# Kernel tuning notes

Hardware: AMD Instinct MI355X
Metric: run time of the kernel (lower is better)

## Reference

```python
import jax, jax.numpy as jnp
import numpy as np

NUM_EMBEDDINGS = 1024
EMBEDDING_DIM = 256
COMMITMENT_COST = 0.25
B = 65536


def setup_inputs() -> dict:
    key = jax.random.key(0)
    k1, k2 = jax.random.split(key)
    inputs = jax.random.normal(k1, (B, EMBEDDING_DIM), dtype=jnp.float32)
    # torch init: uniform(-1/K, 1/K)
    W = jax.random.uniform(k2, (NUM_EMBEDDINGS, EMBEDDING_DIM), dtype=jnp.float32,
                           minval=-1.0 / NUM_EMBEDDINGS, maxval=1.0 / NUM_EMBEDDINGS)
    return {"inputs": inputs, "W": W}


def reference(inputs, W):
    x = inputs  # (B, D)
    # squared L2 distances to every codebook entry: (B, K)
    distances = (jnp.sum(x * x, axis=1, keepdims=True)
                 + jnp.sum(W * W, axis=1)
                 - 2.0 * jnp.matmul(x, W.T))
    idx = jnp.argmin(distances, axis=1)  # (B,)
    # one-hot @ W is just a gather
    quantized = jnp.take(W, idx, axis=0)  # (B, D)

    sg = jax.lax.stop_gradient
    e_latent_loss = jnp.mean((sg(quantized) - x) ** 2)
    q_latent_loss = jnp.mean((quantized - sg(x)) ** 2)
    loss = q_latent_loss + COMMITMENT_COST * e_latent_loss

    # perplexity from code-usage histogram (mean of one-hot rows)
    counts = jax.ops.segment_sum(jnp.ones((x.shape[0],), dtype=x.dtype), idx,
                                 num_segments=NUM_EMBEDDINGS)
    avg_probs = counts / x.shape[0]
    perplexity = jnp.exp(-jnp.sum(avg_probs * jnp.log(avg_probs + 1e-10)))

    # straight-through estimator
    quantized_st = x + sg(quantized - x)
    return quantized_st, loss, perplexity
```

## Files before the change

### kernel.cpp

```cpp
#include <hip/hip_runtime.h>


using h16   = _Float16;
using h16x8 = __attribute__((ext_vector_type(8))) _Float16;
using f32x4 = __attribute__((ext_vector_type(4))) float;

#define W_SCALE 1024.0f
#define W_UNSCALE2 0.001953125f
#define XS_STRIDE 264

__global__ __launch_bounds__(64) void vq_wconv(const float* __restrict__ W,
                                               h16* __restrict__ Whp,
                                               float* __restrict__ wws,
                                               int* __restrict__ zero_base) {
  const int t = threadIdx.x;
  if (blockIdx.x == 0) {
#pragma unroll
    for (int i = t; i < 1088; i += 64) zero_base[i] = 0;
  }
  const int code = blockIdx.x * 2 + (t >> 5);
  const int j = t & 31;
  const int d0 = j * 8;
  f32x4 v0 = *(const f32x4*)(W + (size_t)code * 256 + d0);
  f32x4 v1 = *(const f32x4*)(W + (size_t)code * 256 + d0 + 4);
  h16x8 h;
  h[0] = (h16)(v0[0] * W_SCALE); h[1] = (h16)(v0[1] * W_SCALE);
  h[2] = (h16)(v0[2] * W_SCALE); h[3] = (h16)(v0[3] * W_SCALE);
  h[4] = (h16)(v1[0] * W_SCALE); h[5] = (h16)(v1[1] * W_SCALE);
  h[6] = (h16)(v1[2] * W_SCALE); h[7] = (h16)(v1[3] * W_SCALE);
  const int tile = code >> 4, ks = j >> 2, quad = j & 3, lm = code & 15;
  *(h16x8*)(Whp + (size_t)(((tile * 8 + ks) * 64 + quad * 16 + lm) * 8)) = h;
  float ss = v0[0] * v0[0] + v0[1] * v0[1] + v0[2] * v0[2] + v0[3] * v0[3]
           + v1[0] * v1[0] + v1[1] * v1[1] + v1[2] * v1[2] + v1[3] * v1[3];
#pragma unroll
  for (int m = 1; m <= 16; m <<= 1) ss += __shfl_xor(ss, m);
  if (j == 0) wws[code] = ss;
}

__global__ __launch_bounds__(256, 8) void vq_main(const float* __restrict__ X,
                                                  const h16* __restrict__ Whp,
                                                  const float* __restrict__ wws,
                                                  const float* __restrict__ W,
                                                  float* __restrict__ out,
                                                  float* __restrict__ loss_sum,
                                                  int* __restrict__ counts) {
  __shared__ h16 Xs[32 * XS_STRIDE];
  __shared__ float redS[4 * 32];
  __shared__ int redC[4 * 32];
  __shared__ int sIdx[32];
  __shared__ float xnorm[32];
  const int tid = threadIdx.x;
  const int lane = tid & 63;
  const int wid = tid >> 6;
  const int lm = lane & 15;
  const int quad = lane >> 4;
  const int rowBase = blockIdx.x * 32;

#pragma unroll
  for (int it = 0; it < 4; ++it) {
    int q = it * 256 + tid;
    int r = q >> 5;
    int dp = (q & 31) << 3;
    const float* src = X + (size_t)(rowBase + r) * 256 + dp;
    f32x4 v0 = __builtin_nontemporal_load((const f32x4*)src);
    f32x4 v1 = __builtin_nontemporal_load((const f32x4*)src + 1);
    h16x8 h;
    h[0] = (h16)v0[0]; h[1] = (h16)v0[1]; h[2] = (h16)v0[2]; h[3] = (h16)v0[3];
    h[4] = (h16)v1[0]; h[5] = (h16)v1[1]; h[6] = (h16)v1[2]; h[7] = (h16)v1[3];
    *(h16x8*)(Xs + r * XS_STRIDE + dp) = h;
    float ss = v0[0] * v0[0] + v0[1] * v0[1] + v0[2] * v0[2] + v0[3] * v0[3]
             + v1[0] * v1[0] + v1[1] * v1[1] + v1[2] * v1[2] + v1[3] * v1[3];
#pragma unroll
    for (int m = 1; m <= 16; m <<= 1) ss += __shfl_xor(ss, m);
    if ((q & 31) == 0) xnorm[r] = ss;
  }
  __syncthreads();

  float bestS[8];
  int bestC[8];
#pragma unroll
  for (int s = 0; s < 8; ++s) { bestS[s] = 3.4e38f; bestC[s] = 0x7fffffff; }

  for (int chunk = 0; chunk < 8; ++chunk) {
    const int tbase = chunk * 8 + wid * 2;
    const h16* bptr = Whp + (size_t)tbase * 4096 + lane * 8;
    float wn0 = wws[tbase * 16 + lm];
    float wn1 = wws[tbase * 16 + 16 + lm];
    f32x4 acc[2][2];
#pragma unroll
    for (int mt = 0; mt < 2; ++mt)
#pragma unroll
      for (int nt = 0; nt < 2; ++nt) {
        f32x4 z = {0.0f, 0.0f, 0.0f, 0.0f};
        acc[mt][nt] = z;
      }

#pragma unroll 2
    for (int ks = 0; ks < 8; ++ks) {
      h16x8 b0 = *(const h16x8*)(bptr + ks * 512);
      h16x8 b1 = *(const h16x8*)(bptr + ks * 512 + 4096);
      const int doff = ks * 32 + quad * 8;
#pragma unroll
      for (int mt = 0; mt < 2; ++mt) {
        h16x8 a = *(const h16x8*)(Xs + (mt * 16 + lm) * XS_STRIDE + doff);
        acc[mt][0] = __builtin_amdgcn_mfma_f32_16x16x32_f16(a, b0, acc[mt][0], 0, 0, 0);
        acc[mt][1] = __builtin_amdgcn_mfma_f32_16x16x32_f16(a, b1, acc[mt][1], 0, 0, 0);
      }
    }

#pragma unroll
    for (int nt = 0; nt < 2; ++nt) {
      int code = (tbase + nt) * 16 + lm;
      float wn = nt ? wn1 : wn0;
#pragma unroll
      for (int mt = 0; mt < 2; ++mt)
#pragma unroll
        for (int reg = 0; reg < 4; ++reg) {
          float s = fmaf(-W_UNSCALE2, acc[mt][nt][reg], wn);
          int slot = mt * 4 + reg;
          if (s < bestS[slot]) { bestS[slot] = s; bestC[slot] = code; }
        }
    }
  }

#pragma unroll
  for (int m = 1; m <= 8; m <<= 1) {
#pragma unroll
    for (int s = 0; s < 8; ++s) {
      float os = __shfl_xor(bestS[s], m);
      int oc = __shfl_xor(bestC[s], m);
      if (os < bestS[s] || (os == bestS[s] && oc < bestC[s])) { bestS[s] = os; bestC[s] = oc; }
    }
  }
  if (lm == 0) {
#pragma unroll
    for (int s = 0; s < 8; ++s) {
      int row = (s >> 2) * 16 + quad * 4 + (s & 3);
      redS[wid * 32 + row] = bestS[s];
      redC[wid * 32 + row] = bestC[s];
    }
  }
  __syncthreads();
  if (wid == 0) {
    float lossv = 0.0f;
    if (lane < 32) {
      float b = 3.4e38f;
      int c = 0x7fffffff;
#pragma unroll
      for (int w = 0; w < 4; ++w) {
        float s = redS[w * 32 + lane];
        int cc = redC[w * 32 + lane];
        if (s < b || (s == b && cc < c)) { b = s; c = cc; }
      }
      sIdx[lane] = c;
      atomicAdd(&counts[c], 1);
      lossv = xnorm[lane] + b;
    }
#pragma unroll
    for (int m = 1; m <= 32; m <<= 1) lossv += __shfl_xor(lossv, m);
    if (lane == 0) atomicAdd(loss_sum, lossv);
  }
  __syncthreads();

  const int d4 = lane << 2;
#pragma unroll 2
  for (int i = 0; i < 8; ++i) {
    int row = wid * 8 + i;
    int idx = sIdx[row];
    f32x4 qv = *(const f32x4*)(W + (size_t)idx * 256 + d4);
    __builtin_nontemporal_store(qv, (f32x4*)(out + (size_t)(rowBase + row) * 256 + d4));
  }
}

__global__ __launch_bounds__(256) void vq_finalize(const int* __restrict__ counts,
                                                   const float* __restrict__ loss_sum,
                                                   float* __restrict__ out) {
  __shared__ float red[256];
  const int tid = threadIdx.x;
  float h = 0.0f;
#pragma unroll
  for (int k = tid; k < 1024; k += 256) {
    float p = (float)counts[k] * (1.0f / 65536.0f);
    h += p * logf(p + 1e-10f);
  }
  red[tid] = h;
  __syncthreads();
#pragma unroll
  for (int s = 128; s > 0; s >>= 1) {
    if (tid < s) red[tid] += red[tid + s];
    __syncthreads();
  }
  if (tid == 0) {
    out[16777216] = loss_sum[0] * (1.25f / 16777216.0f);
    out[16777217] = expf(-red[0]);
  }
}

extern "C" void kernel_launch(void* const* d_in, const int* in_sizes, int n_in,
                              void* d_out, int out_size, void* d_ws, size_t ws_size,
                              hipStream_t stream) {
  (void)in_sizes; (void)n_in; (void)out_size; (void)ws_size;
  const float* X = (const float*)d_in[0];
  const float* W = (const float*)d_in[1];
  float* out = (float*)d_out;
  char* ws = (char*)d_ws;
  float* loss_sum = (float*)ws;
  int* counts = (int*)(ws + 256);
  float* wws = (float*)(ws + 4352);
  h16* Whp = (h16*)(ws + 8448);

  vq_wconv<<<512, 64, 0, stream>>>(W, Whp, wws, (int*)ws);
  vq_main<<<2048, 256, 0, stream>>>(X, Whp, wws, W, out, loss_sum, counts);
  vq_finalize<<<1, 256, 0, stream>>>(counts, loss_sum, out);
}
```

Before: 182.5 us.

## Widen per-wave code tile to four N-tiles and store X in MFMA fragment layout

Each wave now processes four 16-code tiles per chunk instead of two, so every A fragment read from shared memory feeds four MFMAs and chunk-loop overhead halves. X is stored in LDS already laid out per MFMA fragment, so lanes read contiguous 16-byte vectors without stride arithmetic. Nontemporal loads and stores are replaced with plain ones, and launch bounds drop to 4 blocks per SIMD to leave room for the larger accumulator set. This raises register pressure and lowers occupancy.

```diff
diff --git a/kernel.cpp b/kernel.cpp
--- a/kernel.cpp
+++ b/kernel.cpp
@@ -7,7 +7,7 @@
 
 #define W_SCALE 1024.0f
 #define W_UNSCALE2 0.001953125f
-#define XS_STRIDE 264
+#define FRAG_H 520
 
 __global__ __launch_bounds__(64) void vq_wconv(const float* __restrict__ W,
                                                h16* __restrict__ Whp,
@@ -37,14 +37,14 @@
   if (j == 0) wws[code] = ss;
 }
 
-__global__ __launch_bounds__(256, 8) void vq_main(const float* __restrict__ X,
+__global__ __launch_bounds__(256, 4) void vq_main(const float* __restrict__ X,
                                                   const h16* __restrict__ Whp,
                                                   const float* __restrict__ wws,
                                                   const float* __restrict__ W,
                                                   float* __restrict__ out,
                                                   float* __restrict__ loss_sum,
                                                   int* __restrict__ counts) {
-  __shared__ h16 Xs[32 * XS_STRIDE];
+  __shared__ h16 Xs[16 * FRAG_H];
   __shared__ float redS[4 * 32];
   __shared__ int redC[4 * 32];
   __shared__ int sIdx[32];
@@ -62,12 +62,13 @@
     int r = q >> 5;
     int dp = (q & 31) << 3;
     const float* src = X + (size_t)(rowBase + r) * 256 + dp;
-    f32x4 v0 = __builtin_nontemporal_load((const f32x4*)src);
-    f32x4 v1 = __builtin_nontemporal_load((const f32x4*)src + 1);
+    f32x4 v0 = *(const f32x4*)src;
+    f32x4 v1 = *(const f32x4*)(src + 4);
     h16x8 h;
     h[0] = (h16)v0[0]; h[1] = (h16)v0[1]; h[2] = (h16)v0[2]; h[3] = (h16)v0[3];
     h[4] = (h16)v1[0]; h[5] = (h16)v1[1]; h[6] = (h16)v1[2]; h[7] = (h16)v1[3];
-    *(h16x8*)(Xs + r * XS_STRIDE + dp) = h;
+    int mt = r >> 4, lmr = r & 15, ksw = dp >> 5, qdw = (dp >> 3) & 3;
+    *(h16x8*)(Xs + (mt * 8 + ksw) * FRAG_H + (qdw * 16 + lmr) * 8) = h;
     float ss = v0[0] * v0[0] + v0[1] * v0[1] + v0[2] * v0[2] + v0[3] * v0[3]
              + v1[0] * v1[0] + v1[1] * v1[1] + v1[2] * v1[2] + v1[3] * v1[3];
 #pragma unroll
@@ -81,37 +82,44 @@
 #pragma unroll
   for (int s = 0; s < 8; ++s) { bestS[s] = 3.4e38f; bestC[s] = 0x7fffffff; }
 
-  for (int chunk = 0; chunk < 8; ++chunk) {
-    const int tbase = chunk * 8 + wid * 2;
-    const h16* bptr = Whp + (size_t)tbase * 4096 + lane * 8;
+  for (int chunk = 0; chunk < 4; ++chunk) {
+    const int tbase = chunk * 16 + wid * 4;
+    const h16* bp = Whp + (size_t)tbase * 4096 + lane * 8;
     float wn0 = wws[tbase * 16 + lm];
     float wn1 = wws[tbase * 16 + 16 + lm];
-    f32x4 acc[2][2];
+    float wn2 = wws[tbase * 16 + 32 + lm];
+    float wn3 = wws[tbase * 16 + 48 + lm];
+    f32x4 acc[2][4];
 #pragma unroll
     for (int mt = 0; mt < 2; ++mt)
 #pragma unroll
-      for (int nt = 0; nt < 2; ++nt) {
+      for (int nt = 0; nt < 4; ++nt) {
         f32x4 z = {0.0f, 0.0f, 0.0f, 0.0f};
         acc[mt][nt] = z;
       }
 
 #pragma unroll 2
     for (int ks = 0; ks < 8; ++ks) {
-      h16x8 b0 = *(const h16x8*)(bptr + ks * 512);
-      h16x8 b1 = *(const h16x8*)(bptr + ks * 512 + 4096);
-      const int doff = ks * 32 + quad * 8;
-#pragma unroll
-      for (int mt = 0; mt < 2; ++mt) {
-        h16x8 a = *(const h16x8*)(Xs + (mt * 16 + lm) * XS_STRIDE + doff);
-        acc[mt][0] = __builtin_amdgcn_mfma_f32_16x16x32_f16(a, b0, acc[mt][0], 0, 0, 0);
-        acc[mt][1] = __builtin_amdgcn_mfma_f32_16x16x32_f16(a, b1, acc[mt][1], 0, 0, 0);
-      }
-    }
-
-#pragma unroll
-    for (int nt = 0; nt < 2; ++nt) {
+      h16x8 b0 = *(const h16x8*)(bp + ks * 512);
+      h16x8 b1 = *(const h16x8*)(bp + ks * 512 + 4096);
+      h16x8 b2 = *(const h16x8*)(bp + ks * 512 + 8192);
+      h16x8 b3 = *(const h16x8*)(bp + ks * 512 + 12288);
+      h16x8 a0 = *(const h16x8*)(Xs + ks * FRAG_H + lane * 8);
+      h16x8 a1 = *(const h16x8*)(Xs + (8 + ks) * FRAG_H + lane * 8);
+      acc[0][0] = __builtin_amdgcn_mfma_f32_16x16x32_f16(a0, b0, acc[0][0], 0, 0, 0);
+      acc[0][1] = __builtin_amdgcn_mfma_f32_16x16x32_f16(a0, b1, acc[0][1], 0, 0, 0);
+      acc[0][2] = __builtin_amdgcn_mfma_f32_16x16x32_f16(a0, b2, acc[0][2], 0, 0, 0);
+      acc[0][3] = __builtin_amdgcn_mfma_f32_16x16x32_f16(a0, b3, acc[0][3], 0, 0, 0);
+      acc[1][0] = __builtin_amdgcn_mfma_f32_16x16x32_f16(a1, b0, acc[1][0], 0, 0, 0);
+      acc[1][1] = __builtin_amdgcn_mfma_f32_16x16x32_f16(a1, b1, acc[1][1], 0, 0, 0);
+      acc[1][2] = __builtin_amdgcn_mfma_f32_16x16x32_f16(a1, b2, acc[1][2], 0, 0, 0);
+      acc[1][3] = __builtin_amdgcn_mfma_f32_16x16x32_f16(a1, b3, acc[1][3], 0, 0, 0);
+    }
+
+#pragma unroll
+    for (int nt = 0; nt < 4; ++nt) {
       int code = (tbase + nt) * 16 + lm;
-      float wn = nt ? wn1 : wn0;
+      float wn = (nt == 0) ? wn0 : (nt == 1) ? wn1 : (nt == 2) ? wn2 : wn3;
 #pragma unroll
       for (int mt = 0; mt < 2; ++mt)
 #pragma unroll
@@ -168,7 +176,7 @@
     int row = wid * 8 + i;
     int idx = sIdx[row];
     f32x4 qv = *(const f32x4*)(W + (size_t)idx * 256 + d4);
-    __builtin_nontemporal_store(qv, (f32x4*)(out + (size_t)(rowBase + row) * 256 + d4));
+    *(f32x4*)(out + (size_t)(rowBase + row) * 256 + d4) = qv;
   }
 }
 
```

New measurement: 179.3 us. About the same (-1.8%).
